# Optimization experiments

Measured on AMD Instinct MI355X. Metric: run time of the kernel, lower is better.

The kernel has to match this reference:

```python
import jax, jax.numpy as jnp
import numpy as np
import math

B, N, D = 4, 2048, 512
H, DH = 8, 128
INNER = H * DH


def setup_inputs() -> dict:
    key = jax.random.key(0)
    k1, k2, k3, k4 = jax.random.split(key, 4)
    x = jax.random.normal(k1, (B, N, D), dtype=jnp.float32)
    Wg = jax.random.normal(k2, (D, INNER), dtype=jnp.float32) * (1.0 / math.sqrt(D))
    Wout = jax.random.normal(k3, (INNER, D), dtype=jnp.float32) * (1.0 / math.sqrt(INNER))
    sigma = jax.random.uniform(k4, (1, H, 1, 1), dtype=jnp.float32, minval=0.5, maxval=2.5)
    return {"x": x, "Wg": Wg, "Wout": Wout, "sigma": sigma}


def reference(x, Wg, Wout, sigma):
    b, n, d = x.shape
    h, dh = H, DH
    # value projection: [b,n,d] @ [d, h*dh] -> [b,h,n,dh]
    v = (x @ Wg).reshape(b, n, h, dh).transpose(0, 2, 1, 3)
    # fixed Gaussian positional mask, shared across batch: build once per head
    pos = jnp.arange(1, n + 1, dtype=jnp.float32)
    diffs = jnp.abs(pos[:, None] - pos[None, :])  # [n, n]
    sig = sigma.reshape(h, 1, 1)  # [h,1,1]
    inv_norm = 1.0 / (jnp.sqrt(2.0 * jnp.float32(math.pi)) * sig)
    gauss = inv_norm * jnp.exp(-(diffs[None] ** 2) / (2.0 * sig ** 2))  # [h,n,n]
    corr = gauss / gauss.sum(-1, keepdims=True)  # row-normalized [h,n,n]
    # attention: broadcast mask over batch
    attn = jnp.einsum('hnm,bhmd->bhnd', corr, v)
    out = attn.transpose(0, 2, 1, 3).reshape(b, n, h * dh)
    return out @ Wout  # dropout p=0.0 -> identity
```

## Files before the change

kernel.cpp:

```cpp
#include <hip/hip_runtime.h>
#include <hip/hip_bf16.h>
#include <math.h>

#define B_ 4
#define N_ 2048
#define D_ 512
#define H_ 8
#define DH_ 128
#define INNER_ 1024
#define W_ 32
#define M_ (B_ * N_)

typedef __attribute__((ext_vector_type(8))) short short8;
typedef __attribute__((ext_vector_type(4))) float floatx4;

typedef const __attribute__((address_space(1))) char* gcp;
typedef __attribute__((address_space(3))) char* lcp;

__device__ __forceinline__ float bf16hi_to_f(unsigned u) {
    union { unsigned u; float f; } c; c.u = u; return c.f;
}

template <typename OutT>
__global__ __launch_bounds__(256, 4) void gemm_bf16_mfma64(
    const __hip_bfloat16* __restrict__ A, const __hip_bfloat16* __restrict__ Bt,
    OutT* __restrict__ C, int M, int N, int K)
{
    __shared__ char smem[16384];
    __hip_bfloat16* Asm = (__hip_bfloat16*)smem;
    __hip_bfloat16* Bsm = (__hip_bfloat16*)(smem + 8192);

    const int tid  = threadIdx.x;
    const int lane = tid & 63;
    const int w    = tid >> 6;
    const int wm   = w >> 1;
    const int wn   = w & 1;
    const int bm   = blockIdx.y;
    const int bn   = blockIdx.x;

    const int kh = lane >> 4;
    const int ml = lane & 15;

    floatx4 acc[2][2];
    #pragma unroll
    for (int i = 0; i < 2; ++i)
        #pragma unroll
        for (int j = 0; j < 2; ++j) acc[i][j] = (floatx4){0.f, 0.f, 0.f, 0.f};

    const char* Ab = (const char*)(A + (size_t)(bm * 64) * K);
    const char* Bb = (const char*)(Bt + (size_t)(bn * 64) * K);
    const size_t rowstride = (size_t)K * 2;

    for (int k0 = 0; k0 < K; k0 += 64) {
        #pragma unroll
        for (int it = 0; it < 2; ++it) {
            int o = it * 4096 + tid * 16;
            int r = o >> 7;
            int s = (o >> 4) & 7;
            int c = s ^ (r & 7);
            size_t goff = (size_t)r * rowstride + (size_t)k0 * 2 + c * 16;
            __builtin_amdgcn_global_load_lds((gcp)(Ab + goff), (lcp)((char*)Asm + o), 16, 0, 0);
            __builtin_amdgcn_global_load_lds((gcp)(Bb + goff), (lcp)((char*)Bsm + o), 16, 0, 0);
        }
        __syncthreads();

        const short* As = (const short*)Asm;
        const short* Bs = (const short*)Bsm;
        short8 af[2][2], bf[2][2];
        #pragma unroll
        for (int t = 0; t < 2; ++t) {
            int ra = wm * 32 + t * 16 + ml;
            int rb = wn * 32 + t * 16 + ml;
            #pragma unroll
            for (int kk = 0; kk < 2; ++kk) {
                int ch = kk * 4 + kh;
                af[t][kk] = *(const short8*)(As + ra * 64 + ((ch ^ (ra & 7)) * 8));
                bf[t][kk] = *(const short8*)(Bs + rb * 64 + ((ch ^ (rb & 7)) * 8));
            }
        }
        #pragma unroll
        for (int kk = 0; kk < 2; ++kk)
            #pragma unroll
            for (int i = 0; i < 2; ++i)
                #pragma unroll
                for (int j = 0; j < 2; ++j)
                    acc[i][j] = __builtin_amdgcn_mfma_f32_16x16x32_bf16(
                        af[i][kk], bf[j][kk], acc[i][j], 0, 0, 0);
        __syncthreads();
    }

    float* Cs = (float*)smem;
    const int rq = lane >> 4;
    const int cl = lane & 15;
    #pragma unroll
    for (int i = 0; i < 2; ++i)
        #pragma unroll
        for (int j = 0; j < 2; ++j)
            #pragma unroll
            for (int r = 0; r < 4; ++r)
                Cs[(wm * 32 + i * 16 + rq * 4 + r) * 64 + wn * 32 + j * 16 + cl] = acc[i][j][r];
    __syncthreads();

    if constexpr (sizeof(OutT) == 2) {
        int row = tid >> 3;
        #pragma unroll
        for (int p = 0; p < 2; ++p) {
            int idx = p * 256 + tid;
            int rr = idx >> 3;
            int cc = (idx & 7) * 8;
            const float* src = Cs + rr * 64 + cc;
            __hip_bfloat16 o[8];
            #pragma unroll
            for (int e = 0; e < 8; ++e) o[e] = __float2bfloat16(src[e]);
            *(short8*)((__hip_bfloat16*)C + (size_t)(bm * 64 + rr) * N + bn * 64 + cc) = *(short8*)o;
        }
        (void)row;
    } else {
        #pragma unroll
        for (int p = 0; p < 4; ++p) {
            int idx = p * 256 + tid;
            int rr = idx >> 4;
            int cc = (idx & 15) * 4;
            float4 vv = *(const float4*)(Cs + rr * 64 + cc);
            *(float4*)((float*)C + (size_t)(bm * 64 + rr) * N + bn * 64 + cc) = vv;
        }
    }
}

__device__ __forceinline__ void transpose32(
    const float* __restrict__ src, __hip_bfloat16* __restrict__ dst,
    int R, int Cn, int rt, int ct, int tid)
{
    __shared__ float t[32][33];
    int c0 = ct * 32, r0 = rt * 32;
    int lx = tid & 31, ly = tid >> 5;
    #pragma unroll
    for (int i = 0; i < 32; i += 8)
        t[ly + i][lx] = src[(size_t)(r0 + ly + i) * Cn + c0 + lx];
    __syncthreads();
    #pragma unroll
    for (int i = 0; i < 32; i += 8)
        dst[(size_t)(c0 + ly + i) * R + r0 + lx] = __float2bfloat16(t[lx][ly + i]);
}

__global__ __launch_bounds__(256) void prep(
    const float* __restrict__ x, const float* __restrict__ Wg,
    const float* __restrict__ Wout, __hip_bfloat16* __restrict__ x_bf,
    __hip_bfloat16* __restrict__ Wg_t, __hip_bfloat16* __restrict__ Wout_t)
{
    const int bid = blockIdx.x;
    const int tid = threadIdx.x;
    if (bid < 2048) {
        int i = bid * 256 + tid;
        const float4* s = (const float4*)x + (size_t)i * 2;
        float4 a = s[0], b = s[1];
        __hip_bfloat16 o[8] = {
            __float2bfloat16(a.x), __float2bfloat16(a.y), __float2bfloat16(a.z), __float2bfloat16(a.w),
            __float2bfloat16(b.x), __float2bfloat16(b.y), __float2bfloat16(b.z), __float2bfloat16(b.w)};
        *(short8*)(x_bf + (size_t)i * 8) = *(short8*)o;
    } else if (bid < 2560) {
        int id2 = bid - 2048;
        transpose32(Wg, Wg_t, D_, INNER_, id2 >> 5, id2 & 31, tid);
    } else {
        int id2 = bid - 2560;
        transpose32(Wout, Wout_t, INNER_, D_, id2 >> 4, id2 & 15, tid);
    }
}

#define TNA 64
#define ROWSB (TNA + 2 * W_)
#define CHB 64

struct bf16x4s { __hip_bfloat16 a, b, c, d; };

__global__ __launch_bounds__(256) void banded_attn3(
    const __hip_bfloat16* __restrict__ v, const float* __restrict__ sigma,
    __hip_bfloat16* __restrict__ attn)
{
    __shared__ __hip_bfloat16 vs[ROWSB][CHB];
    __shared__ float wtab[2 * W_ + 1];
    __shared__ float winv[TNA];

    const int tid = threadIdx.x;
    const int n0  = blockIdx.x * TNA;
    const int h   = blockIdx.y >> 1;
    const int ch0 = (blockIdx.y & 1) * CHB;
    const int b   = blockIdx.z;

    const __hip_bfloat16* vbase = v + (size_t)b * N_ * INNER_ + h * DH_ + ch0;
    #pragma unroll
    for (int it = 0; it < 4; ++it) {
        int idx = tid + it * 256;
        int r = idx >> 3;
        int g = idx & 7;
        int m = n0 - W_ + r;
        int4 val = make_int4(0, 0, 0, 0);
        if (m >= 0 && m < N_) val = *(const int4*)(vbase + (size_t)m * INNER_ + g * 8);
        *(int4*)&vs[r][g * 8] = val;
    }
    if (tid <= 2 * W_) {
        float sig = sigma[h];
        float d = (float)(tid - W_);
        wtab[tid] = __expf(-d * d / (2.0f * sig * sig));
    }
    __syncthreads();

    if (tid < TNA) {
        int n = n0 + tid;
        float ws = 0.f;
        #pragma unroll
        for (int j = 0; j <= 2 * W_; ++j) {
            int m = n - W_ + j;
            ws += (m >= 0 && m < N_) ? wtab[j] : 0.f;
        }
        winv[tid] = 1.0f / ws;
    }
    __syncthreads();

    const int cg = tid & 15;
    const int rg = tid >> 4;

    float4 acc[4];
    #pragma unroll
    for (int r = 0; r < 4; ++r) acc[r] = make_float4(0.f, 0.f, 0.f, 0.f);
    float wreg[4] = {0.f, 0.f, 0.f, 0.f};

    const unsigned* vrow0 = (const unsigned*)&vs[rg * 4][cg * 4];

    #pragma unroll 4
    for (int l = 0; l < 2 * W_ + 4; ++l) {
        wreg[l & 3] = (l <= 2 * W_) ? wtab[l] : 0.f;
        const unsigned* p = vrow0 + (size_t)l * (CHB / 2);
        unsigned r0 = p[0], r1 = p[1];
        float4 vv;
        vv.x = bf16hi_to_f(r0 << 16);
        vv.y = bf16hi_to_f(r0 & 0xffff0000u);
        vv.z = bf16hi_to_f(r1 << 16);
        vv.w = bf16hi_to_f(r1 & 0xffff0000u);
        #pragma unroll
        for (int r = 0; r < 4; ++r) {
            float wgt = wreg[(l - r) & 3];
            acc[r].x += wgt * vv.x; acc[r].y += wgt * vv.y;
            acc[r].z += wgt * vv.z; acc[r].w += wgt * vv.w;
        }
    }

    #pragma unroll
    for (int r = 0; r < 4; ++r) {
        int nl = rg * 4 + r;
        float s = winv[nl];
        bf16x4s o = { __float2bfloat16(acc[r].x * s), __float2bfloat16(acc[r].y * s),
                      __float2bfloat16(acc[r].z * s), __float2bfloat16(acc[r].w * s) };
        *(bf16x4s*)(attn + ((size_t)b * N_ + n0 + nl) * INNER_ + h * DH_ + ch0 + cg * 4) = o;
    }
}

extern "C" void kernel_launch(void* const* d_in, const int* in_sizes, int n_in,
                              void* d_out, int out_size, void* d_ws, size_t ws_size,
                              hipStream_t stream) {
    const float* x     = (const float*)d_in[0];
    const float* Wg    = (const float*)d_in[1];
    const float* Wout  = (const float*)d_in[2];
    const float* sigma = (const float*)d_in[3];
    float* out = (float*)d_out;

    char* ws = (char*)d_ws;
    __hip_bfloat16* x_bf   = (__hip_bfloat16*)ws;
    __hip_bfloat16* Wg_t   = (__hip_bfloat16*)(ws + (((size_t)8)  << 20));
    __hip_bfloat16* Wout_t = (__hip_bfloat16*)(ws + (((size_t)9)  << 20));
    __hip_bfloat16* v_bf   = (__hip_bfloat16*)(ws + (((size_t)10) << 20));
    __hip_bfloat16* attn   = (__hip_bfloat16*)(ws + (((size_t)26) << 20));

    prep<<<dim3(3072), dim3(256), 0, stream>>>(x, Wg, Wout, x_bf, Wg_t, Wout_t);

    gemm_bf16_mfma64<__hip_bfloat16><<<dim3(INNER_ / 64, M_ / 64), dim3(256), 0, stream>>>(
        x_bf, Wg_t, v_bf, M_, INNER_, D_);

    banded_attn3<<<dim3(N_ / TNA, H_ * 2, B_), dim3(256), 0, stream>>>(v_bf, sigma, attn);

    gemm_bf16_mfma64<float><<<dim3(D_ / 64, M_ / 64), dim3(256), 0, stream>>>(
        attn, Wout_t, out, M_, D_, INNER_);
}
```

Before: 137.0 us.

## Fuse four launches into one persistent kernel with grid-wide barriers

Replaces the prep, projection GEMM, banded blur and output GEMM launches with a single 1024-block kernel that runs each stage as device functions, separated by atomic-counter grid barriers. Each block handles a fixed share of tiles per stage, and the barrier counters are zeroed with a memset before launch. The goal is to remove per-launch overhead and the gaps between kernels. The cost is barrier spin time and fixed tile assignment. It also relies on all 1024 blocks being co-resident, otherwise the barriers deadlock.

```diff
diff --git a/kernel.cpp b/kernel.cpp
--- a/kernel.cpp
+++ b/kernel.cpp
@@ -10,6 +10,7 @@
 #define INNER_ 1024
 #define W_ 32
 #define M_ (B_ * N_)
+#define GRID_ 1024
 
 typedef __attribute__((ext_vector_type(8))) short short8;
 typedef __attribute__((ext_vector_type(4))) float floatx4;
@@ -21,25 +22,49 @@
     union { unsigned u; float f; } c; c.u = u; return c.f;
 }
 
+__device__ __forceinline__ void gbar(unsigned* c) {
+    __syncthreads();
+    if (threadIdx.x == 0) {
+        __threadfence();
+        __hip_atomic_fetch_add(c, 1u, __ATOMIC_ACQ_REL, __HIP_MEMORY_SCOPE_AGENT);
+        while (__hip_atomic_load(c, __ATOMIC_ACQUIRE, __HIP_MEMORY_SCOPE_AGENT) < GRID_)
+            __builtin_amdgcn_s_sleep(1);
+        __threadfence();
+    }
+    __syncthreads();
+}
+
+__device__ __forceinline__ void transpose32(
+    const float* __restrict__ src, __hip_bfloat16* __restrict__ dst,
+    int R, int Cn, int rt, int ct, int tid, char* smem)
+{
+    float (*t)[33] = (float(*)[33])smem;
+    int c0 = ct * 32, r0 = rt * 32;
+    int lx = tid & 31, ly = tid >> 5;
+    #pragma unroll
+    for (int i = 0; i < 32; i += 8)
+        t[ly + i][lx] = src[(size_t)(r0 + ly + i) * Cn + c0 + lx];
+    __syncthreads();
+    #pragma unroll
+    for (int i = 0; i < 32; i += 8)
+        dst[(size_t)(c0 + ly + i) * R + r0 + lx] = __float2bfloat16(t[lx][ly + i]);
+    __syncthreads();
+}
+
 template <typename OutT>
-__global__ __launch_bounds__(256, 4) void gemm_bf16_mfma64(
+__device__ __forceinline__ void gemm_tile(
     const __hip_bfloat16* __restrict__ A, const __hip_bfloat16* __restrict__ Bt,
-    OutT* __restrict__ C, int M, int N, int K)
+    OutT* __restrict__ C, int N, int K, int bm, int bn, int tid, char* smem)
 {
-    __shared__ char smem[16384];
     __hip_bfloat16* Asm = (__hip_bfloat16*)smem;
     __hip_bfloat16* Bsm = (__hip_bfloat16*)(smem + 8192);
 
-    const int tid  = threadIdx.x;
     const int lane = tid & 63;
     const int w    = tid >> 6;
     const int wm   = w >> 1;
     const int wn   = w & 1;
-    const int bm   = blockIdx.y;
-    const int bn   = blockIdx.x;
-
-    const int kh = lane >> 4;
-    const int ml = lane & 15;
+    const int kh   = lane >> 4;
+    const int ml   = lane & 15;
 
     floatx4 acc[2][2];
     #pragma unroll
@@ -102,7 +127,6 @@
     __syncthreads();
 
     if constexpr (sizeof(OutT) == 2) {
-        int row = tid >> 3;
         #pragma unroll
         for (int p = 0; p < 2; ++p) {
             int idx = p * 256 + tid;
@@ -114,7 +138,6 @@
             for (int e = 0; e < 8; ++e) o[e] = __float2bfloat16(src[e]);
             *(short8*)((__hip_bfloat16*)C + (size_t)(bm * 64 + rr) * N + bn * 64 + cc) = *(short8*)o;
         }
-        (void)row;
     } else {
         #pragma unroll
         for (int p = 0; p < 4; ++p) {
@@ -125,46 +148,7 @@
             *(float4*)((float*)C + (size_t)(bm * 64 + rr) * N + bn * 64 + cc) = vv;
         }
     }
-}
-
-__device__ __forceinline__ void transpose32(
-    const float* __restrict__ src, __hip_bfloat16* __restrict__ dst,
-    int R, int Cn, int rt, int ct, int tid)
-{
-    __shared__ float t[32][33];
-    int c0 = ct * 32, r0 = rt * 32;
-    int lx = tid & 31, ly = tid >> 5;
-    #pragma unroll
-    for (int i = 0; i < 32; i += 8)
-        t[ly + i][lx] = src[(size_t)(r0 + ly + i) * Cn + c0 + lx];
-    __syncthreads();
-    #pragma unroll
-    for (int i = 0; i < 32; i += 8)
-        dst[(size_t)(c0 + ly + i) * R + r0 + lx] = __float2bfloat16(t[lx][ly + i]);
-}
-
-__global__ __launch_bounds__(256) void prep(
-    const float* __restrict__ x, const float* __restrict__ Wg,
-    const float* __restrict__ Wout, __hip_bfloat16* __restrict__ x_bf,
-    __hip_bfloat16* __restrict__ Wg_t, __hip_bfloat16* __restrict__ Wout_t)
-{
-    const int bid = blockIdx.x;
-    const int tid = threadIdx.x;
-    if (bid < 2048) {
-        int i = bid * 256 + tid;
-        const float4* s = (const float4*)x + (size_t)i * 2;
-        float4 a = s[0], b = s[1];
-        __hip_bfloat16 o[8] = {
-            __float2bfloat16(a.x), __float2bfloat16(a.y), __float2bfloat16(a.z), __float2bfloat16(a.w),
-            __float2bfloat16(b.x), __float2bfloat16(b.y), __float2bfloat16(b.z), __float2bfloat16(b.w)};
-        *(short8*)(x_bf + (size_t)i * 8) = *(short8*)o;
-    } else if (bid < 2560) {
-        int id2 = bid - 2048;
-        transpose32(Wg, Wg_t, D_, INNER_, id2 >> 5, id2 & 31, tid);
-    } else {
-        int id2 = bid - 2560;
-        transpose32(Wout, Wout_t, INNER_, D_, id2 >> 4, id2 & 15, tid);
-    }
+    __syncthreads();
 }
 
 #define TNA 64
@@ -173,19 +157,19 @@
 
 struct bf16x4s { __hip_bfloat16 a, b, c, d; };
 
-__global__ __launch_bounds__(256) void banded_attn3(
+__device__ __forceinline__ void blur_tile(
     const __hip_bfloat16* __restrict__ v, const float* __restrict__ sigma,
-    __hip_bfloat16* __restrict__ attn)
+    __hip_bfloat16* __restrict__ attn, int job, int tid, char* smem)
 {
-    __shared__ __hip_bfloat16 vs[ROWSB][CHB];
-    __shared__ float wtab[2 * W_ + 1];
-    __shared__ float winv[TNA];
-
-    const int tid = threadIdx.x;
-    const int n0  = blockIdx.x * TNA;
-    const int h   = blockIdx.y >> 1;
-    const int ch0 = (blockIdx.y & 1) * CHB;
-    const int b   = blockIdx.z;
+    __hip_bfloat16 (*vs)[CHB] = (__hip_bfloat16(*)[CHB])smem;
+    float* wtab = (float*)(smem + 16384);
+    float* winv = wtab + 68;
+
+    const int b   = job >> 9;
+    const int y   = (job >> 5) & 15;
+    const int n0  = (job & 31) * TNA;
+    const int h   = y >> 1;
+    const int ch0 = (y & 1) * CHB;
 
     const __hip_bfloat16* vbase = v + (size_t)b * N_ * INNER_ + h * DH_ + ch0;
     #pragma unroll
@@ -253,6 +237,54 @@
                       __float2bfloat16(acc[r].z * s), __float2bfloat16(acc[r].w * s) };
         *(bf16x4s*)(attn + ((size_t)b * N_ + n0 + nl) * INNER_ + h * DH_ + ch0 + cg * 4) = o;
     }
+    __syncthreads();
+}
+
+__global__ __launch_bounds__(256, 4) void mega(
+    const float* __restrict__ x, const float* __restrict__ Wg,
+    const float* __restrict__ Wout, const float* __restrict__ sigma,
+    float* __restrict__ out,
+    __hip_bfloat16* __restrict__ x_bf, __hip_bfloat16* __restrict__ Wg_t,
+    __hip_bfloat16* __restrict__ Wout_t, __hip_bfloat16* __restrict__ v_bf,
+    __hip_bfloat16* __restrict__ attn, unsigned* __restrict__ bar)
+{
+    __shared__ char smem[17408];
+    const int bid = blockIdx.x;
+    const int tid = threadIdx.x;
+
+    {
+        #pragma unroll
+        for (int p = 0; p < 2; ++p) {
+            int g = bid * 512 + p * 256 + tid;
+            const float4* s = (const float4*)x + (size_t)g * 2;
+            float4 a = s[0], bb = s[1];
+            __hip_bfloat16 o[8] = {
+                __float2bfloat16(a.x),  __float2bfloat16(a.y),  __float2bfloat16(a.z),  __float2bfloat16(a.w),
+                __float2bfloat16(bb.x), __float2bfloat16(bb.y), __float2bfloat16(bb.z), __float2bfloat16(bb.w)};
+            *(short8*)(x_bf + (size_t)g * 8) = *(short8*)o;
+        }
+        if (bid < 512) {
+            transpose32(Wg, Wg_t, D_, INNER_, bid >> 5, bid & 31, tid, smem);
+        } else {
+            int id2 = bid - 512;
+            transpose32(Wout, Wout_t, INNER_, D_, id2 >> 4, id2 & 15, tid, smem);
+        }
+    }
+    gbar(bar + 0);
+
+    #pragma unroll
+    for (int t2 = 0; t2 < 2; ++t2) {
+        int j = bid + t2 * 1024;
+        gemm_tile<__hip_bfloat16>(x_bf, Wg_t, v_bf, INNER_, D_, j >> 4, j & 15, tid, smem);
+    }
+    gbar(bar + 16);
+
+    #pragma unroll
+    for (int t2 = 0; t2 < 2; ++t2)
+        blur_tile(v_bf, sigma, attn, bid * 2 + t2, tid, smem);
+    gbar(bar + 32);
+
+    gemm_tile<float>(attn, Wout_t, out, D_, INNER_, bid >> 3, bid & 7, tid, smem);
 }
 
 extern "C" void kernel_launch(void* const* d_in, const int* in_sizes, int n_in,
@@ -270,14 +302,9 @@
     __hip_bfloat16* Wout_t = (__hip_bfloat16*)(ws + (((size_t)9)  << 20));
     __hip_bfloat16* v_bf   = (__hip_bfloat16*)(ws + (((size_t)10) << 20));
     __hip_bfloat16* attn   = (__hip_bfloat16*)(ws + (((size_t)26) << 20));
-
-    prep<<<dim3(3072), dim3(256), 0, stream>>>(x, Wg, Wout, x_bf, Wg_t, Wout_t);
-
-    gemm_bf16_mfma64<__hip_bfloat16><<<dim3(INNER_ / 64, M_ / 64), dim3(256), 0, stream>>>(
-        x_bf, Wg_t, v_bf, M_, INNER_, D_);
-
-    banded_attn3<<<dim3(N_ / TNA, H_ * 2, B_), dim3(256), 0, stream>>>(v_bf, sigma, attn);
-
-    gemm_bf16_mfma64<float><<<dim3(D_ / 64, M_ / 64), dim3(256), 0, stream>>>(
-        attn, Wout_t, out, M_, D_, INNER_);
-}
+    unsigned*       bar    = (unsigned*)(ws + (((size_t)60) << 20));
+
+    hipMemsetAsync(bar, 0, 192, stream);
+    mega<<<dim3(GRID_), dim3(256), 0, stream>>>(
+        x, Wg, Wout, sigma, out, x_bf, Wg_t, Wout_t, v_bf, attn, bar);
+}
```

Result: slower. 513.4 us (+274.9%).
